# Kernel tuning notes

Measured on AMD Instinct MI355X. Metric: run time of the kernel, lower is better.

## Reference

```python
import jax, jax.numpy as jnp
import numpy as np
import math

LMAX = 3
_EPS = 1e-7


def _np_J(ell):
    """Precompute J^l = diag((-1)^i) @ d^l(pi/2) in float64 numpy (constant)."""
    if ell == 0:
        return np.ones((1, 1))
    c = math.cos(math.pi / 4.0)
    s = math.sin(math.pi / 4.0)
    fact = [1.0]
    for i in range(1, 2 * ell + 2):
        fact.append(fact[-1] * i)
    dim = 2 * ell + 1
    d = np.zeros((dim, dim))
    for mi in range(dim):
        m = ell - mi
        for mpi in range(dim):
            mp = ell - mpi
            pref = math.sqrt(fact[ell + m] * fact[ell - m] * fact[ell + mp] * fact[ell - mp])
            val = 0.0
            for k in range(max(0, m - mp), min(ell + m, ell - mp) + 1):
                denom = fact[ell + m - k] * fact[ell - mp - k] * fact[k + mp - m] * fact[k]
                val += ((-1) ** (m - mp + k)) * pref / denom * c ** (2 * ell + mp - m - 2 * k) * s ** (m - mp + 2 * k)
            d[mi, mpi] = val
    signs = np.array([(-1) ** i for i in range(dim)])
    return signs[:, None] * d


_J_MATS = [_np_J(ell) for ell in range(LMAX + 1)]


def _z_rot(angle, ell):
    """Real-SH z-rotation matrix [E, 2l+1, 2l+1]; m ordered l..-l.
    Z[i, rev(i)] = sin(m_i*phi), Z[i, i] = cos(m_i*phi) (diag set last so m=0 cell = cos(0)=1)."""
    dim = 2 * ell + 1
    m = jnp.arange(ell, -ell - 1, -1, dtype=angle.dtype)  # [dim]
    idx = np.arange(dim)
    rev = idx[::-1].copy()
    Z = jnp.zeros((angle.shape[0], dim, dim), dtype=angle.dtype)
    ph = angle[:, None] * m  # [E, dim]
    Z = Z.at[:, idx, rev].set(jnp.sin(ph))
    Z = Z.at[:, idx, idx].set(jnp.cos(ph))
    return Z


def reference(edge_vec):
    """Per-edge block-diagonal Wigner D (ZYZ, D^l = Z(a) J Z(b) J Z(g)).
    edge_vec: [E, 3] -> [E, (LMAX+1)^2, (LMAX+1)^2]."""
    dtype = edge_vec.dtype
    x, y, z = edge_vec[:, 0], edge_vec[:, 1], edge_vec[:, 2]
    r = jnp.sqrt(jnp.sum(edge_vec * edge_vec, axis=-1))
    cos_beta = jnp.clip(z / jnp.maximum(r, _EPS), -1.0 + _EPS, 1.0 - _EPS)  # safe acos
    beta = jnp.arccos(cos_beta)
    degenerate = (jnp.abs(x) < _EPS) & (jnp.abs(y) < _EPS)  # safe atan2
    x_safe = jnp.where(degenerate, jnp.ones_like(x), x)
    alpha = jnp.where(degenerate, jnp.zeros_like(x), jnp.arctan2(y, x_safe))
    gamma = jnp.zeros_like(alpha)

    E = edge_vec.shape[0]
    full_dim = (LMAX + 1) ** 2
    out = jnp.zeros((E, full_dim, full_dim), dtype=dtype)
    off = 0
    for ell in range(LMAX + 1):
        dim = 2 * ell + 1
        J = jnp.asarray(_J_MATS[ell], dtype=dtype)  # [dim, dim]
        Za = _z_rot(alpha, ell)
        Zb = _z_rot(beta, ell)
        Zg = _z_rot(gamma, ell)
        Dl = Za @ J @ Zb @ J @ Zg  # [E, dim, dim]
        out = out.at[:, off:off + dim, off:off + dim].set(Dl)
        off += dim
    return out


def setup_inputs() -> dict:
    key = jax.random.key(0)
    edge_vec = jax.random.normal(key, (400000, 3), dtype=jnp.float32)
    return {"edge_vec": edge_vec}
```

## Files before the change

### kernel.cpp

```cpp
#include <hip/hip_runtime.h>
#include <math.h>

typedef float vfloat4 __attribute__((ext_vector_type(4)));

constexpr double csqrt(double a) {
    double x = a > 1.0 ? a : 1.0;
    for (int i = 0; i < 48; ++i) x = 0.5 * (x + a / x);
    return x;
}

constexpr double j_entry_d(int ell, int mi, int mpi) {
    if (ell == 0) return 1.0;
    double fact[8] = {1.0, 1.0, 2.0, 6.0, 24.0, 120.0, 720.0, 5040.0};
    int m  = ell - mi;
    int mp = ell - mpi;
    double pref  = csqrt(fact[ell + m] * fact[ell - m] * fact[ell + mp] * fact[ell - mp]);
    double scale = 1.0 / (double)(1 << ell);
    int k0 = (m - mp) > 0 ? (m - mp) : 0;
    int k1 = (ell + m) < (ell - mp) ? (ell + m) : (ell - mp);
    double val = 0.0;
    for (int k = k0; k <= k1; ++k) {
        double denom = fact[ell + m - k] * fact[ell - mp - k] * fact[k + mp - m] * fact[k];
        double t = pref / denom * scale;
        val += ((m - mp + k) & 1) ? -t : t;
    }
    return (mi & 1) ? -val : val;
}

struct alignas(16) RowTabs { float t[16][68]; };

constexpr RowTabs make_tabs() {
    RowTabs T{};
    for (int il = 0; il < 16; ++il) {
        int L  = (il == 0) ? 0 : (il < 4) ? 1 : (il < 9) ? 2 : 3;
        int li = il - L * L;
        int m_i = L - li;
        int am  = m_i < 0 ? -m_i : m_i;
        double sgn = (m_i < 0) ? -1.0 : 1.0;
        for (int s = 0; s < 7; ++s) {
            int ms  = 3 - s;
            int ams = ms < 0 ? -ms : ms;
            bool in = (ams <= L);
            int  kp = L - ms;
            T.t[il][s]     = in ? (float)j_entry_d(L, li, kp) : 0.0f;
            T.t[il][7 + s] = in ? (float)(sgn * j_entry_d(L, 2 * L - li, kp)) : 0.0f;
            for (int v = 0; v < 7; ++v)
                T.t[il][14 + 7 * s + v] =
                    (in && v <= 2 * L) ? (float)j_entry_d(L, kp, v) : 0.0f;
        }
        T.t[il][63] = (am == 0) ? 1.0f : 0.0f;
        T.t[il][64] = (am == 1) ? 1.0f : 0.0f;
        T.t[il][65] = (am == 2) ? 1.0f : 0.0f;
        T.t[il][66] = (am == 3) ? 1.0f : 0.0f;
        T.t[il][67] = 0.0f;
    }
    return T;
}

__device__ constexpr RowTabs g_tabs = make_tabs();

__global__ __launch_bounds__(256, 4)
void EdgeRotation_49435073577214_kernel(const float* __restrict__ ev,
                                        float* __restrict__ out,
                                        int E, int nwaves) {
    __shared__ float lds[4][1024];

    const int tid  = (int)threadIdx.x;
    const int lane = tid & 63;
    const int wib  = tid >> 6;
    const int g    = lane >> 4;
    const int il   = lane & 15;
    float* wlds = lds[wib];

    const int gw = (int)blockIdx.x * 4 + wib;

    float jmu[7], jrv[7], M[7][7], sA0, sA1, sA2, sA3;
    {
        const float* tp = g_tabs.t[il];
#pragma unroll
        for (int s = 0; s < 7; ++s) { jmu[s] = tp[s]; jrv[s] = tp[7 + s]; }
#pragma unroll
        for (int s = 0; s < 7; ++s)
#pragma unroll
            for (int v = 0; v < 7; ++v) M[s][v] = tp[14 + 7 * s + v];
        sA0 = tp[63]; sA1 = tp[64]; sA2 = tp[65]; sA3 = tp[66];
    }
    const int LL = (il == 0) ? 0 : (il < 4) ? 1 : (il < 9) ? 4 : 9;
    float* pS = wlds + g * 256 + il * 16 + LL;

    {
        vfloat4 zz; zz.x = 0.f; zz.y = 0.f; zz.z = 0.f; zz.w = 0.f;
        vfloat4* wv4 = reinterpret_cast<vfloat4*>(wlds);
        wv4[lane]       = zz;
        wv4[lane + 64]  = zz;
        wv4[lane + 128] = zz;
        wv4[lane + 192] = zz;
    }

    const int Em1 = E - 1;
    for (int e0 = 4 * gw; e0 < E; e0 += 4 * nwaves) {
        int eg = e0 + g;
        eg = eg < E ? eg : Em1;

        const float x = ev[3 * eg], y = ev[3 * eg + 1], z = ev[3 * eg + 2];

        const float xx   = x * x;
        const float r2   = fmaf(z, z, fmaf(y, y, xx));
        const float rho2 = fmaf(y, y, xx);
        const float rinv = __builtin_amdgcn_rsqf(fmaxf(r2, 1e-30f));
        float cbv = z * rinv;
        cbv = fminf(fmaxf(cbv, -1.0f + 1e-7f), 1.0f - 1e-7f);
        const float sbv = __builtin_amdgcn_sqrtf(fmaxf(fmaf(-cbv, cbv, 1.0f), 0.0f));
        const float rhoinv = __builtin_amdgcn_rsqf(fmaxf(rho2, 1e-30f));
        const bool  ndg = rho2 >= 1e-14f;
        const float ca1 = ndg ? x * rhoinv : 1.0f;
        const float sa1 = ndg ? y * rhoinv : 0.0f;

        const float CA2 = fmaf(ca1, ca1, -(sa1 * sa1));
        const float SA2 = 2.0f * ca1 * sa1;
        const float CA3 = fmaf(CA2, ca1, -(SA2 * sa1));
        const float SA3 = fmaf(SA2, ca1, CA2 * sa1);
        const float CB2 = fmaf(cbv, cbv, -(sbv * sbv));
        const float SB2 = 2.0f * cbv * sbv;
        const float CB3 = fmaf(CB2, cbv, -(SB2 * sbv));
        const float SB3 = fmaf(SB2, cbv, CB2 * sbv);

        float ca = fmaf(sA1, ca1, sA0);
        ca = fmaf(sA2, CA2, ca);
        ca = fmaf(sA3, CA3, ca);
        float sa = sA1 * sa1;
        sa = fmaf(sA2, SA2, sa);
        sa = fmaf(sA3, SA3, sa);

        float u[7];
#pragma unroll
        for (int s = 0; s < 7; ++s) u[s] = fmaf(ca, jmu[s], sa * jrv[s]);

        float w[7];
        w[0] = fmaf(-u[6], SB3, u[0] * CB3);
        w[1] = fmaf(-u[5], SB2, u[1] * CB2);
        w[2] = fmaf(-u[4], sbv, u[2] * cbv);
        w[3] = u[3];
        w[4] = fmaf( u[2], sbv, u[4] * cbv);
        w[5] = fmaf( u[1], SB2, u[5] * CB2);
        w[6] = fmaf( u[0], SB3, u[6] * CB3);

#pragma unroll
        for (int v = 0; v < 7; ++v) {
            float d = 0.f;
#pragma unroll
            for (int s = 0; s < 7; ++s) d = fmaf(w[s], M[s][v], d);
            pS[v] = d;
        }

        const vfloat4* rv4 = reinterpret_cast<const vfloat4*>(wlds);
        if (e0 + 4 <= E) {
#pragma unroll
            for (int q = 0; q < 4; ++q) {
                vfloat4 o = rv4[q * 64 + lane];
                reinterpret_cast<vfloat4*>(out)[(size_t)(e0 + q) * 64 + lane] = o;
            }
        } else {
#pragma unroll
            for (int q = 0; q < 4; ++q) {
                if (e0 + q < E) {
                    vfloat4 o = rv4[q * 64 + lane];
                    reinterpret_cast<vfloat4*>(out)[(size_t)(e0 + q) * 64 + lane] = o;
                }
            }
        }
    }
}

extern "C" void kernel_launch(void* const* d_in, const int* in_sizes, int n_in,
                              void* d_out, int out_size, void* d_ws, size_t ws_size,
                              hipStream_t stream) {
    const float* ev  = (const float*)d_in[0];
    float*       out = (float*)d_out;
    int E = in_sizes[0] / 3;

    dim3 grid(2048), block(256);
    int nwaves = (int)((2048 * 256) / 64);
    hipLaunchKernelGGL(EdgeRotation_49435073577214_kernel, grid, block, 0, stream,
                       ev, out, E, nwaves);
}
```

Baseline: 86.30 us.

## Prefetch edge coords into LDS, double-buffer staging, use nontemporal stores

Each wave now loads all of its edge coordinates into LDS up front with coalesced reads, instead of issuing scattered global loads every iteration. The LDS staging buffer is doubled and the loop is unrolled by two, so consecutive iterations write separate buffers and can overlap. Output writes become nontemporal stores to reduce cache pollution on the large streaming output. The coordinate buffer is capped at 16 iterations per wave, so inputs with more edges than the grid can cover in 16 iterations would overflow it, and the LDS footprint per block grows.

Result: no change. 85.25 us (-1.2%).

```diff
diff --git a/kernel.cpp b/kernel.cpp
--- a/kernel.cpp
+++ b/kernel.cpp
@@ -59,20 +59,35 @@
 
 __device__ constexpr RowTabs g_tabs = make_tabs();
 
+#define MAX_IT 16
+
 __global__ __launch_bounds__(256, 4)
 void EdgeRotation_49435073577214_kernel(const float* __restrict__ ev,
                                         float* __restrict__ out,
                                         int E, int nwaves) {
-    __shared__ float lds[4][1024];
+    __shared__ float ldsD[4][2048];
+    __shared__ float ldsC[4][12 * MAX_IT];
 
     const int tid  = (int)threadIdx.x;
     const int lane = tid & 63;
     const int wib  = tid >> 6;
     const int g    = lane >> 4;
     const int il   = lane & 15;
-    float* wlds = lds[wib];
+    float* wlds = ldsD[wib];
+    float* wcrd = ldsC[wib];
 
     const int gw = (int)blockIdx.x * 4 + wib;
+
+    const int span = 4 * nwaves;
+    int nit = 0;
+    if (4 * gw < E) nit = (E - 4 * gw + span - 1) / span;
+
+    const int ncf = nit * 12;
+    for (int t = lane; t < ncf; t += 64) {
+        const int it = t / 12, j = t - 12 * it;
+        const long long fidx = 3LL * (4 * gw + (long long)span * it) + j;
+        wcrd[t] = (fidx < 3LL * E) ? ev[fidx] : 0.0f;
+    }
 
     float jmu[7], jrv[7], M[7][7], sA0, sA1, sA2, sA3;
     {
@@ -91,85 +106,91 @@
     {
         vfloat4 zz; zz.x = 0.f; zz.y = 0.f; zz.z = 0.f; zz.w = 0.f;
         vfloat4* wv4 = reinterpret_cast<vfloat4*>(wlds);
-        wv4[lane]       = zz;
-        wv4[lane + 64]  = zz;
-        wv4[lane + 128] = zz;
-        wv4[lane + 192] = zz;
-    }
-
-    const int Em1 = E - 1;
-    for (int e0 = 4 * gw; e0 < E; e0 += 4 * nwaves) {
-        int eg = e0 + g;
-        eg = eg < E ? eg : Em1;
-
-        const float x = ev[3 * eg], y = ev[3 * eg + 1], z = ev[3 * eg + 2];
-
-        const float xx   = x * x;
-        const float r2   = fmaf(z, z, fmaf(y, y, xx));
-        const float rho2 = fmaf(y, y, xx);
-        const float rinv = __builtin_amdgcn_rsqf(fmaxf(r2, 1e-30f));
-        float cbv = z * rinv;
-        cbv = fminf(fmaxf(cbv, -1.0f + 1e-7f), 1.0f - 1e-7f);
-        const float sbv = __builtin_amdgcn_sqrtf(fmaxf(fmaf(-cbv, cbv, 1.0f), 0.0f));
-        const float rhoinv = __builtin_amdgcn_rsqf(fmaxf(rho2, 1e-30f));
-        const bool  ndg = rho2 >= 1e-14f;
-        const float ca1 = ndg ? x * rhoinv : 1.0f;
-        const float sa1 = ndg ? y * rhoinv : 0.0f;
-
-        const float CA2 = fmaf(ca1, ca1, -(sa1 * sa1));
-        const float SA2 = 2.0f * ca1 * sa1;
-        const float CA3 = fmaf(CA2, ca1, -(SA2 * sa1));
-        const float SA3 = fmaf(SA2, ca1, CA2 * sa1);
-        const float CB2 = fmaf(cbv, cbv, -(sbv * sbv));
-        const float SB2 = 2.0f * cbv * sbv;
-        const float CB3 = fmaf(CB2, cbv, -(SB2 * sbv));
-        const float SB3 = fmaf(SB2, cbv, CB2 * sbv);
-
-        float ca = fmaf(sA1, ca1, sA0);
-        ca = fmaf(sA2, CA2, ca);
-        ca = fmaf(sA3, CA3, ca);
-        float sa = sA1 * sa1;
-        sa = fmaf(sA2, SA2, sa);
-        sa = fmaf(sA3, SA3, sa);
-
-        float u[7];
-#pragma unroll
-        for (int s = 0; s < 7; ++s) u[s] = fmaf(ca, jmu[s], sa * jrv[s]);
-
-        float w[7];
-        w[0] = fmaf(-u[6], SB3, u[0] * CB3);
-        w[1] = fmaf(-u[5], SB2, u[1] * CB2);
-        w[2] = fmaf(-u[4], sbv, u[2] * cbv);
-        w[3] = u[3];
-        w[4] = fmaf( u[2], sbv, u[4] * cbv);
-        w[5] = fmaf( u[1], SB2, u[5] * CB2);
-        w[6] = fmaf( u[0], SB3, u[6] * CB3);
-
-#pragma unroll
-        for (int v = 0; v < 7; ++v) {
-            float d = 0.f;
-#pragma unroll
-            for (int s = 0; s < 7; ++s) d = fmaf(w[s], M[s][v], d);
-            pS[v] = d;
-        }
-
-        const vfloat4* rv4 = reinterpret_cast<const vfloat4*>(wlds);
-        if (e0 + 4 <= E) {
-#pragma unroll
-            for (int q = 0; q < 4; ++q) {
-                vfloat4 o = rv4[q * 64 + lane];
-                reinterpret_cast<vfloat4*>(out)[(size_t)(e0 + q) * 64 + lane] = o;
-            }
-        } else {
-#pragma unroll
-            for (int q = 0; q < 4; ++q) {
-                if (e0 + q < E) {
-                    vfloat4 o = rv4[q * 64 + lane];
-                    reinterpret_cast<vfloat4*>(out)[(size_t)(e0 + q) * 64 + lane] = o;
-                }
-            }
-        }
-    }
+#pragma unroll
+        for (int q = 0; q < 8; ++q) wv4[lane + 64 * q] = zz;
+    }
+
+    const vfloat4* rv4 = reinterpret_cast<const vfloat4*>(wlds);
+
+#define BODY(ITV, PAR)                                                         \
+    do {                                                                       \
+        const int e0 = 4 * gw + span * (ITV);                                  \
+        const float x = wcrd[(ITV) * 12 + 3 * g + 0];                          \
+        const float y = wcrd[(ITV) * 12 + 3 * g + 1];                          \
+        const float z = wcrd[(ITV) * 12 + 3 * g + 2];                          \
+        const float xx   = x * x;                                              \
+        const float r2   = fmaf(z, z, fmaf(y, y, xx));                         \
+        const float rho2 = fmaf(y, y, xx);                                     \
+        const float rinv = __builtin_amdgcn_rsqf(fmaxf(r2, 1e-30f));           \
+        float cbv = z * rinv;                                                  \
+        cbv = fminf(fmaxf(cbv, -1.0f + 1e-7f), 1.0f - 1e-7f);                  \
+        const float sbv =                                                      \
+            __builtin_amdgcn_sqrtf(fmaxf(fmaf(-cbv, cbv, 1.0f), 0.0f));        \
+        const float rhoinv = __builtin_amdgcn_rsqf(fmaxf(rho2, 1e-30f));       \
+        const bool  ndg = rho2 >= 1e-14f;                                      \
+        const float ca1 = ndg ? x * rhoinv : 1.0f;                             \
+        const float sa1 = ndg ? y * rhoinv : 0.0f;                             \
+        const float CA2 = fmaf(ca1, ca1, -(sa1 * sa1));                        \
+        const float SA2 = 2.0f * ca1 * sa1;                                    \
+        const float CA3 = fmaf(CA2, ca1, -(SA2 * sa1));                        \
+        const float SA3 = fmaf(SA2, ca1, CA2 * sa1);                           \
+        const float CB2 = fmaf(cbv, cbv, -(sbv * sbv));                        \
+        const float SB2 = 2.0f * cbv * sbv;                                    \
+        const float CB3 = fmaf(CB2, cbv, -(SB2 * sbv));                        \
+        const float SB3 = fmaf(SB2, cbv, CB2 * sbv);                           \
+        float ca = fmaf(sA1, ca1, sA0);                                        \
+        ca = fmaf(sA2, CA2, ca);                                               \
+        ca = fmaf(sA3, CA3, ca);                                               \
+        float sa = sA1 * sa1;                                                  \
+        sa = fmaf(sA2, SA2, sa);                                               \
+        sa = fmaf(sA3, SA3, sa);                                               \
+        float u[7];                                                            \
+        _Pragma("unroll")                                                      \
+        for (int s = 0; s < 7; ++s) u[s] = fmaf(ca, jmu[s], sa * jrv[s]);      \
+        float w[7];                                                            \
+        w[0] = fmaf(-u[6], SB3, u[0] * CB3);                                   \
+        w[1] = fmaf(-u[5], SB2, u[1] * CB2);                                   \
+        w[2] = fmaf(-u[4], sbv, u[2] * cbv);                                   \
+        w[3] = u[3];                                                           \
+        w[4] = fmaf( u[2], sbv, u[4] * cbv);                                   \
+        w[5] = fmaf( u[1], SB2, u[5] * CB2);                                   \
+        w[6] = fmaf( u[0], SB3, u[6] * CB3);                                   \
+        _Pragma("unroll")                                                      \
+        for (int v = 0; v < 7; ++v) {                                          \
+            float d = 0.f;                                                     \
+            _Pragma("unroll")                                                  \
+            for (int s = 0; s < 7; ++s) d = fmaf(w[s], M[s][v], d);            \
+            pS[(PAR) * 1024 + v] = d;                                          \
+        }                                                                      \
+        if (e0 + 4 <= E) {                                                     \
+            _Pragma("unroll")                                                  \
+            for (int q = 0; q < 4; ++q) {                                      \
+                vfloat4 o = rv4[(PAR) * 256 + q * 64 + lane];                  \
+                __builtin_nontemporal_store(o,                                 \
+                    reinterpret_cast<vfloat4*>(out) +                          \
+                    (size_t)(e0 + q) * 64 + lane);                             \
+            }                                                                  \
+        } else {                                                               \
+            _Pragma("unroll")                                                  \
+            for (int q = 0; q < 4; ++q) {                                      \
+                if (e0 + q < E) {                                              \
+                    vfloat4 o = rv4[(PAR) * 256 + q * 64 + lane];              \
+                    __builtin_nontemporal_store(o,                             \
+                        reinterpret_cast<vfloat4*>(out) +                      \
+                        (size_t)(e0 + q) * 64 + lane);                         \
+                }                                                              \
+            }                                                                  \
+        }                                                                      \
+    } while (0)
+
+    int it = 0;
+    for (; it + 2 <= nit; it += 2) {
+        BODY(it, 0);
+        BODY(it + 1, 1);
+    }
+    if (it < nit) BODY(it, 0);
+
+#undef BODY
 }
 
 extern "C" void kernel_launch(void* const* d_in, const int* in_sizes, int n_in,
```
